# Performance work log

Measured on AMD Instinct MI355X. Metric: run time of the kernel, lower is better.

The kernel has to match this reference:

```python
import jax, jax.numpy as jnp
import numpy as np

NUM_HEADS = 32
NUM_KV = 8
HEAD_DIM = 128


def rotate_half(x):
    half = x.shape[-1] // 2
    x1, x2 = x[..., :half], x[..., half:]
    return jnp.concatenate([-x2, x1], axis=-1)


def apply_rope(x, cos, sin):
    # x: [B, H, S, D]; cos/sin: [S, D] broadcast over batch and heads
    return x * cos + rotate_half(x) * sin


def setup_inputs() -> dict:
    key = jax.random.key(0)
    kx, kqkv, kout = jax.random.split(key, 3)
    B, S, H = 2, 2048, 4096
    x = jax.random.normal(kx, (B, S, H), dtype=jnp.float32)
    Wqkv = jax.random.normal(kqkv, (H, NUM_HEADS * HEAD_DIM + 2 * NUM_KV * HEAD_DIM), dtype=jnp.float32) * (H ** -0.5)
    Wout = jax.random.normal(kout, (H, H), dtype=jnp.float32) * (H ** -0.5)
    # realistic RoPE tables (seq, head_dim)
    inv_freq = 1.0 / (10000.0 ** (np.arange(0, HEAD_DIM, 2, dtype=np.float32) / HEAD_DIM))
    freqs = np.outer(np.arange(S, dtype=np.float32), inv_freq)  # [S, D/2]
    emb = np.concatenate([freqs, freqs], axis=-1)  # [S, D]
    cos = jnp.asarray(np.cos(emb), dtype=jnp.float32)
    sin = jnp.asarray(np.sin(emb), dtype=jnp.float32)
    return {"x": x, "cos": cos, "sin": sin, "Wqkv": Wqkv, "Wout": Wout}


def reference(x, cos, sin, Wqkv, Wout):
    B, S, H = x.shape
    nh, nkv, hd = NUM_HEADS, NUM_KV, HEAD_DIM
    qkv = x @ Wqkv  # [B, S, (nh+2*nkv)*hd]
    q, k, v = jnp.split(qkv, [nh * hd, nh * hd + nkv * hd], axis=-1)
    q = q.reshape(B, S, nh, hd).transpose(0, 2, 1, 3)   # [B, nh, S, hd]
    k = k.reshape(B, S, nkv, hd).transpose(0, 2, 1, 3)  # [B, nkv, S, hd]
    v = v.reshape(B, S, nkv, hd).transpose(0, 2, 1, 3)
    q = apply_rope(q, cos, sin)
    k = apply_rope(k, cos, sin)
    group = nh // nkv
    k = jnp.repeat(k, group, axis=1)  # repeat_interleave over head dim
    v = jnp.repeat(v, group, axis=1)
    scale = 1.0 / jnp.sqrt(jnp.asarray(hd, dtype=x.dtype))
    scores = jnp.einsum('bhqd,bhkd->bhqk', q, k) * scale  # [B, nh, S, S]
    causal = jnp.triu(jnp.ones((S, S), dtype=bool), k=1)
    scores = jnp.where(causal, -jnp.inf, scores)
    w = jax.nn.softmax(scores, axis=-1)
    out = jnp.einsum('bhqk,bhkd->bhqd', w, v)  # [B, nh, S, hd]
    out = out.transpose(0, 2, 1, 3).reshape(B, S, nh * hd)
    return out @ Wout
```

## Files before the change

kernel.cpp:

```cpp
#include <hip/hip_runtime.h>

typedef unsigned short u16;
typedef __attribute__((ext_vector_type(8))) short s16x8;
typedef __attribute__((ext_vector_type(4))) short s16x4;
typedef __attribute__((ext_vector_type(4))) float f32x4;

#define DEVI __device__ __forceinline__

DEVI u16 f2b(float f) {
  union { float f; unsigned u; } v; v.f = f;
  unsigned r = v.u + 0x7FFFu + ((v.u >> 16) & 1u);
  return (u16)(r >> 16);
}
DEVI float b2f(u16 h) {
  union { unsigned u; float f; } v; v.u = ((unsigned)h) << 16;
  return v.f;
}

typedef const __attribute__((address_space(1))) void gas_void;
typedef __attribute__((address_space(3))) void las_void;
DEVI void gload16(const void* g, void* l) {
  __builtin_amdgcn_global_load_lds((gas_void*)g, (las_void*)l, 16, 0, 0);
}

__global__ void conv_bf16(const float* __restrict__ in, u16* __restrict__ out, int n8) {
  int i = blockIdx.x * 256 + threadIdx.x;
  if (i >= n8) return;
  const float* p = in + (size_t)i * 8;
  float4 u = *(const float4*)p;
  float4 v = *(const float4*)(p + 4);
  s16x8 o = {(short)f2b(u.x), (short)f2b(u.y), (short)f2b(u.z), (short)f2b(u.w),
             (short)f2b(v.x), (short)f2b(v.y), (short)f2b(v.z), (short)f2b(v.w)};
  *(s16x8*)(out + (size_t)i * 8) = o;
}

__global__ void trans_bf16(const float* __restrict__ W, u16* __restrict__ Wt, int K, int N) {
  __shared__ __attribute__((aligned(16))) u16 tile[64][68];
  const int t = threadIdx.x;
  const int n0 = blockIdx.x * 64, k0 = blockIdx.y * 64;
#pragma unroll
  for (int i = 0; i < 4; ++i) {
    int c = i * 256 + t;
    int r = c >> 4, q = c & 15;
    float4 v = *(const float4*)(W + (size_t)(k0 + r) * N + n0 + q * 4);
    s16x4 o = {(short)f2b(v.x), (short)f2b(v.y), (short)f2b(v.z), (short)f2b(v.w)};
    *(s16x4*)&tile[r][q * 4] = o;
  }
  __syncthreads();
#pragma unroll
  for (int i = 0; i < 2; ++i) {
    int c = i * 256 + t;
    int n_ = c >> 3, ck = (c & 7) * 8;
    s16x8 o;
#pragma unroll
    for (int j = 0; j < 8; ++j) o[j] = (short)tile[ck + j][n_];
    *(s16x8*)(Wt + (size_t)(n0 + n_) * K + k0 + ck) = o;
  }
}

template <typename TC>
__global__ __launch_bounds__(512, 2) void gemm128(const u16* __restrict__ A,
                                                  const u16* __restrict__ Bt,
                                                  TC* __restrict__ C, int M, int N, int K) {
  __shared__ __attribute__((aligned(16))) u16 As[2][128 * 64];
  __shared__ __attribute__((aligned(16))) u16 Bs[2][256 * 64];
  const int t = threadIdx.x;
  const int nbn = N >> 8;
  const int nwg = (M >> 7) * nbn;
  const int chunk = nwg >> 3;
  const int id = (blockIdx.x & 7) * chunk + (blockIdx.x >> 3);
  const int row0 = (id / nbn) << 7, col0 = (id % nbn) << 8;
  const int w = t >> 6, lane = t & 63, lc = lane & 15, lg = lane >> 4;
  const int wm = (w >> 2) * 64;
  const int wn4 = (w & 3);
  const int sw7 = lc & 7;

  const f32x4 FZ = {0.f, 0.f, 0.f, 0.f};
  f32x4 acc[4][4];
#pragma unroll
  for (int i = 0; i < 4; ++i)
#pragma unroll
    for (int j = 0; j < 4; ++j) acc[i][j] = FZ;

  const int ra = t >> 3;
  const int sa = (t & 7) ^ (ra & 7);
  const int bg0 = ((ra >> 5) << 6) | (ra & 31);

#define G1_STG_A(kt, sl)                                                          \
  {                                                                               \
    const u16* ap = A + (size_t)(row0 + ra) * K + ((kt) << 6) + (sa << 3);        \
    gload16(ap, (u16*)As[sl] + t * 8);                                            \
    gload16(ap + (size_t)64 * K, (u16*)As[sl] + (512 + t) * 8);                   \
  }
#define G1_STG_B(kt, H, sl)                                                       \
  {                                                                               \
    const u16* bp = Bt + (size_t)(col0 + bg0 + ((H) << 5)) * K + ((kt) << 6) + (sa << 3); \
    gload16(bp, (u16*)Bs[sl] + (H)*8192 + t * 8);                                 \
    gload16(bp + (size_t)128 * K, (u16*)Bs[sl] + (H)*8192 + (512 + t) * 8);       \
  }
#define G1_LOAD_A(buf)                                                            \
  _Pragma("unroll") for (int mf = 0; mf < 4; ++mf)                                \
  _Pragma("unroll") for (int ks = 0; ks < 2; ++ks)                                \
    af[mf][ks] = *(const s16x8*)(As[buf] + (wm + mf * 16 + lc) * 64 +             \
                                 (((ks * 4 + lg) ^ sw7) << 3));
#define G1_LOAD_B(NH, buf)                                                        \
  _Pragma("unroll") for (int nfl = 0; nfl < 2; ++nfl)                             \
  _Pragma("unroll") for (int ks = 0; ks < 2; ++ks)                                \
    bfv[nfl][ks] = *(const s16x8*)(Bs[buf] + ((NH)*128 + wn4 * 32 + nfl * 16 + lc) * 64 + \
                                   (((ks * 4 + lg) ^ sw7) << 3));
#define G1_MFMA(NH)                                                               \
  _Pragma("unroll") for (int ks = 0; ks < 2; ++ks)                                \
  _Pragma("unroll") for (int mf = 0; mf < 4; ++mf)                                \
  _Pragma("unroll") for (int nfl = 0; nfl < 2; ++nfl)                             \
    acc[mf][(NH)*2 + nfl] = __builtin_amdgcn_mfma_f32_16x16x32_bf16(              \
        af[mf][ks], bfv[nfl][ks], acc[mf][(NH)*2 + nfl], 0, 0, 0);
#define BAR __builtin_amdgcn_s_barrier()
#define PRIO1 __builtin_amdgcn_s_setprio(1)
#define PRIO0 __builtin_amdgcn_s_setprio(0)

  s16x8 af[4][2], bfv[2][2];
  const int NT = K >> 6, TM = NT - 1;

  G1_STG_A(0, 0) G1_STG_B(0, 0, 0) G1_STG_B(0, 1, 0)
  asm volatile("s_waitcnt vmcnt(2)" ::: "memory");
  BAR;

  for (int kt = 0; kt < NT; ++kt) {
    const int buf = kt & 1, nb = buf ^ 1;
    const int tp1 = (kt + 1) & TM;
    G1_LOAD_A(buf)
    G1_LOAD_B(0, buf)
    G1_STG_A(tp1, nb)
    G1_STG_B(tp1, 0, nb)
    BAR; PRIO1; G1_MFMA(0) PRIO0;
    asm volatile("s_waitcnt vmcnt(4)" ::: "memory");
    BAR;
    G1_LOAD_B(1, buf)
    G1_STG_B(tp1, 1, nb)
    BAR; PRIO1; G1_MFMA(1) PRIO0;
    asm volatile("s_waitcnt vmcnt(2)" ::: "memory");
    BAR;
  }
  asm volatile("s_waitcnt vmcnt(0)" ::: "memory");
#undef G1_STG_A
#undef G1_STG_B
#undef G1_LOAD_A
#undef G1_LOAD_B
#undef G1_MFMA
#undef BAR
#undef PRIO1
#undef PRIO0

#pragma unroll
  for (int mf = 0; mf < 4; ++mf)
#pragma unroll
    for (int nf = 0; nf < 4; ++nf)
#pragma unroll
      for (int r = 0; r < 4; ++r) {
        const int rg = row0 + wm + mf * 16 + lg * 4 + r;
        const int cg = col0 + wn4 * 64 + (nf >> 1) * 32 + (nf & 1) * 16 + lc;
        if constexpr (sizeof(TC) == 2)
          ((u16*)C)[(size_t)rg * N + cg] = f2b(acc[mf][nf][r]);
        else
          ((float*)C)[(size_t)rg * N + cg] = acc[mf][nf][r];
      }
}

template <typename TC>
__global__ __launch_bounds__(512, 2) void gemm256(const u16* __restrict__ A,
                                                  const u16* __restrict__ Bt,
                                                  TC* __restrict__ C, int M, int N, int K) {
  __shared__ __attribute__((aligned(16))) u16 As[2][2][128 * 64];
  __shared__ __attribute__((aligned(16))) u16 Bs[2][2][128 * 64];
  const int t = threadIdx.x;
  const int nbn = N >> 8;
  const int nwg = (M >> 8) * nbn;
  const int chunk = nwg >> 3;
  const int id = (blockIdx.x & 7) * chunk + (blockIdx.x >> 3);
  const int row0 = (id / nbn) << 8, col0 = (id % nbn) << 8;
  const int w = t >> 6, lane = t & 63, lc = lane & 15, lg = lane >> 4;
  const int wqm = (w >> 2) * 64;
  const int wqn = (w & 3) * 32;
  const int sw7 = lc & 7;

  const f32x4 FZ = {0.f, 0.f, 0.f, 0.f};
  f32x4 acc[4][4][2];
#pragma unroll
  for (int q = 0; q < 4; ++q)
#pragma unroll
    for (int i = 0; i < 4; ++i)
#pragma unroll
      for (int j = 0; j < 2; ++j) acc[q][i][j] = FZ;

  const int s_r0 = t >> 3, s_r1 = (512 + t) >> 3;
  const int s_s = t & 7;

#define STG_A(kt, H, sl)                                                                   \
  {                                                                                        \
    gload16(A + (size_t)(row0 + (H)*128 + s_r0) * K + ((kt) << 6) + ((s_s ^ (s_r0 & 7)) << 3), \
            (u16*)As[sl][H] + t * 8);                                                      \
    gload16(A + (size_t)(row0 + (H)*128 + s_r1) * K + ((kt) << 6) + ((s_s ^ (s_r1 & 7)) << 3), \
            (u16*)As[sl][H] + (512 + t) * 8);                                              \
  }
#define STG_B(kt, H, sl)                                                                   \
  {                                                                                        \
    gload16(Bt + (size_t)(col0 + (H)*128 + s_r0) * K + ((kt) << 6) + ((s_s ^ (s_r0 & 7)) << 3), \
            (u16*)Bs[sl][H] + t * 8);                                                      \
    gload16(Bt + (size_t)(col0 + (H)*128 + s_r1) * K + ((kt) << 6) + ((s_s ^ (s_r1 & 7)) << 3), \
            (u16*)Bs[sl][H] + (512 + t) * 8);                                              \
  }
#define LOAD_A(MH, buf)                                                           \
  _Pragma("unroll") for (int mf = 0; mf < 4; ++mf)                                \
  _Pragma("unroll") for (int ks = 0; ks < 2; ++ks)                                \
    af[mf][ks] = *(const s16x8*)(As[buf][MH] + (wqm + mf * 16 + lc) * 64 +        \
                                 (((ks * 4 + lg) ^ sw7) << 3));
#define LOAD_B(NH, buf, DST)                                                      \
  _Pragma("unroll") for (int nf = 0; nf < 2; ++nf)                                \
  _Pragma("unroll") for (int ks = 0; ks < 2; ++ks)                                \
    DST[nf][ks] = *(const s16x8*)(Bs[buf][NH] + (wqn + nf * 16 + lc) * 64 +       \
                                  (((ks * 4 + lg) ^ sw7) << 3));
#define MFMA_Q(q, BV)                                                             \
  _Pragma("unroll") for (int ks = 0; ks < 2; ++ks)                                \
  _Pragma("unroll") for (int mf = 0; mf < 4; ++mf)                                \
  _Pragma("unroll") for (int nf = 0; nf < 2; ++nf)                                \
    acc[q][mf][nf] = __builtin_amdgcn_mfma_f32_16x16x32_bf16(                     \
        af[mf][ks], BV[nf][ks], acc[q][mf][nf], 0, 0, 0);
#define BAR __builtin_amdgcn_s_barrier()
#define PRIO1 __builtin_amdgcn_s_setprio(1)
#define PRIO0 __builtin_amdgcn_s_setprio(0)
#define WAIT6 asm volatile("s_waitcnt vmcnt(6)" ::: "memory")

  s16x8 af[4][2], bfv0[2][2], bfv1[2][2];
  const int NT = K >> 6, TM = NT - 1;

  STG_A(0, 0, 0) STG_B(0, 0, 0) STG_B(0, 1, 0) STG_A(0, 1, 0)
  STG_A(1, 0, 1) STG_B(1, 0, 1) STG_B(1, 1, 1)
  WAIT6;
  BAR;

  for (int kt = 0; kt < NT; ++kt) {
    const int buf = kt & 1, nb = buf ^ 1;
    const int tp1 = (kt + 1) & TM, tp2 = (kt + 2) & TM;
    LOAD_A(0, buf) LOAD_B(0, buf, bfv0)
    STG_A(tp1, 1, nb)
    BAR; PRIO1; MFMA_Q(0, bfv0) PRIO0; BAR;
    LOAD_B(1, buf, bfv1)
    STG_A(tp2, 0, buf)
    BAR; PRIO1; MFMA_Q(1, bfv1) PRIO0; BAR;
    LOAD_A(1, buf)
    STG_B(tp2, 0, buf)
    BAR; PRIO1; MFMA_Q(2, bfv1) PRIO0; BAR;
    STG_B(tp2, 1, buf)
    BAR; PRIO1; MFMA_Q(3, bfv0) PRIO0;
    WAIT6;
    BAR;
  }
  asm volatile("s_waitcnt vmcnt(0)" ::: "memory");
  BAR;
#undef STG_A
#undef STG_B
#undef LOAD_A
#undef LOAD_B
#undef MFMA_Q
#undef BAR
#undef PRIO1
#undef PRIO0
#undef WAIT6

  const int qmh[4] = {0, 0, 1, 1}, qnh[4] = {0, 1, 1, 0};
#pragma unroll
  for (int q = 0; q < 4; ++q)
#pragma unroll
    for (int mf = 0; mf < 4; ++mf)
#pragma unroll
      for (int nf = 0; nf < 2; ++nf)
#pragma unroll
        for (int r = 0; r < 4; ++r) {
          const int rg = row0 + qmh[q] * 128 + wqm + mf * 16 + lg * 4 + r;
          const int cg = col0 + qnh[q] * 128 + wqn + nf * 16 + lc;
          if constexpr (sizeof(TC) == 2)
            ((u16*)C)[(size_t)rg * N + cg] = f2b(acc[q][mf][nf][r]);
          else
            ((float*)C)[(size_t)rg * N + cg] = acc[q][mf][nf][r];
        }
}

__global__ void rope_kernel(u16* __restrict__ qkv, const float* __restrict__ cosb,
                            const float* __restrict__ sinb) {
  const int bs = blockIdx.x;
  const int s = bs & 2047;
  u16* row = qkv + (size_t)bs * 6144;
  const float* cr = cosb + s * 128;
  const float* sr = sinb + s * 128;
  for (int p = threadIdx.x; p < 320; p += 256) {
    int head = p >> 3, dc = (p & 7) * 8;
    int ci = head * 128 + dc;
    s16x8 a = *(const s16x8*)&row[ci];
    s16x8 bb = *(const s16x8*)&row[ci + 64];
    float4 c0 = *(const float4*)(cr + dc), c1 = *(const float4*)(cr + dc + 4);
    float4 s0 = *(const float4*)(sr + dc), s1 = *(const float4*)(sr + dc + 4);
    float cv[8] = {c0.x, c0.y, c0.z, c0.w, c1.x, c1.y, c1.z, c1.w};
    float sv[8] = {s0.x, s0.y, s0.z, s0.w, s1.x, s1.y, s1.z, s1.w};
    s16x8 o1, o2;
#pragma unroll
    for (int j = 0; j < 8; ++j) {
      float x1 = b2f((u16)a[j]), x2 = b2f((u16)bb[j]);
      o1[j] = (short)f2b(x1 * cv[j] - x2 * sv[j]);
      o2[j] = (short)f2b(x2 * cv[j] + x1 * sv[j]);
    }
    *(s16x8*)&row[ci] = o1;
    *(s16x8*)&row[ci + 64] = o2;
  }
}

__global__ void vtrans_kernel(const u16* __restrict__ qkv, u16* __restrict__ v_t) {
  __shared__ __attribute__((aligned(16))) u16 tile[64][72];
  const int t = threadIdx.x;
  const int s0 = blockIdx.x * 64;
  const int d0 = blockIdx.y * 64;
  const int bk = blockIdx.z;
  const int b = bk >> 3, kvh = bk & 7;
  const int slot = t & 7, r0 = t >> 3;
#pragma unroll
  for (int i = 0; i < 2; ++i) {
    int s_ = r0 + 32 * i;
    *(s16x8*)&tile[s_][slot * 8] =
        *(const s16x8*)(qkv + (size_t)(b * 2048 + s0 + s_) * 6144 + 5120 + kvh * 128 + d0 + slot * 8);
  }
  __syncthreads();
#pragma unroll
  for (int i = 0; i < 2; ++i) {
    int d_ = r0 + 32 * i;
    s16x8 v;
#pragma unroll
    for (int j = 0; j < 8; ++j) v[j] = (short)tile[slot * 8 + j][d_];
    *(s16x8*)(v_t + ((size_t)bk * 128 + d0 + d_) * 2048 + s0 + slot * 8) = v;
  }
}

__global__ void __launch_bounds__(256, 2) attn_kernel(const u16* __restrict__ qkv,
                                                      const u16* __restrict__ v_t,
                                                      u16* __restrict__ attn) {
  __shared__ __attribute__((aligned(16))) u16 Ks[64][136];
  __shared__ __attribute__((aligned(16))) u16 Vs[128][72];
  __shared__ __attribute__((aligned(16))) u16 Ps[4][32][72];
  const int t = threadIdx.x;
  const int f = blockIdx.x;
  const int xcd = f & 7, ix = f >> 3;
  const int g = (xcd << 1) | (ix >> 6);
  const int r_ = ix & 63;
  const int b = g >> 3, kvh = g & 7;
  const int qt = 15 - (r_ >> 2);
  const int h = kvh * 4 + (r_ & 3);
  const int q0 = qt * 128;
  const int w = t >> 6, lane = t & 63, lc = lane & 15, lg = lane >> 4;
  const int qw = q0 + w * 32;

  const u16* qbase = qkv + (size_t)(b * 2048) * 6144 + h * 128;
  const u16* kbase = qkv + (size_t)(b * 2048) * 6144 + 4096 + kvh * 128;
  const u16* vbase = v_t + (size_t)(b * 8 + kvh) * 128 * 2048;

  s16x8 qf[2][4];
#pragma unroll
  for (int mf = 0; mf < 2; ++mf)
#pragma unroll
    for (int ks = 0; ks < 4; ++ks)
      qf[mf][ks] = *(const s16x8*)(qbase + (size_t)(qw + mf * 16 + lc) * 6144 + ks * 32 + lg * 8);

  const f32x4 FZ = {0.f, 0.f, 0.f, 0.f};
  f32x4 o_acc[2][8];
  float m_run[2][4], l_run[2][4];
#pragma unroll
  for (int mf = 0; mf < 2; ++mf) {
#pragma unroll
    for (int nf = 0; nf < 8; ++nf) o_acc[mf][nf] = FZ;
#pragma unroll
    for (int r = 0; r < 4; ++r) { m_run[mf][r] = -3e38f; l_run[mf][r] = 0.f; }
  }
  const float scale2 = 0.08838834764831845f * 1.44269504088896340736f;

  const int ntiles = q0 / 64 + 2;
  s16x8 kr[4], vr[4];
#pragma unroll
  for (int i = 0; i < 4; ++i) {
    int c = i * 256 + t;
    kr[i] = *(const s16x8*)(kbase + (size_t)(c >> 4) * 6144 + (c & 15) * 8);
    vr[i] = *(const s16x8*)(vbase + (size_t)(c >> 3) * 2048 + (c & 7) * 8);
  }

  for (int kt = 0; kt < ntiles; ++kt) {
    const int k0 = kt * 64;
    __syncthreads();
#pragma unroll
    for (int i = 0; i < 4; ++i) {
      int c = i * 256 + t;
      *(s16x8*)&Ks[c >> 4][(c & 15) * 8] = kr[i];
      *(s16x8*)&Vs[c >> 3][(c & 7) * 8] = vr[i];
    }
    __syncthreads();
    if (kt + 1 < ntiles) {
      int k1 = k0 + 64;
#pragma unroll
      for (int i = 0; i < 4; ++i) {
        int c = i * 256 + t;
        kr[i] = *(const s16x8*)(kbase + (size_t)(k1 + (c >> 4)) * 6144 + (c & 15) * 8);
        vr[i] = *(const s16x8*)(vbase + (size_t)(c >> 3) * 2048 + k1 + (c & 7) * 8);
      }
    }
    if (k0 > qw + 31) continue;

    f32x4 sacc[2][4];
#pragma unroll
    for (int mf = 0; mf < 2; ++mf)
#pragma unroll
      for (int nf = 0; nf < 4; ++nf) sacc[mf][nf] = FZ;
#pragma unroll
    for (int ks = 0; ks < 4; ++ks) {
      s16x8 kf[4];
#pragma unroll
      for (int nf = 0; nf < 4; ++nf)
        kf[nf] = *(const s16x8*)&Ks[nf * 16 + lc][ks * 32 + lg * 8];
#pragma unroll
      for (int mf = 0; mf < 2; ++mf)
#pragma unroll
        for (int nf = 0; nf < 4; ++nf)
          sacc[mf][nf] = __builtin_amdgcn_mfma_f32_16x16x32_bf16(qf[mf][ks], kf[nf], sacc[mf][nf], 0, 0, 0);
    }

#pragma unroll
    for (int mf = 0; mf < 2; ++mf) {
      float pm[4] = {-3e38f, -3e38f, -3e38f, -3e38f};
      const bool dm = (k0 + 63 > qw + mf * 16);
      if (dm) {
#pragma unroll
        for (int nf = 0; nf < 4; ++nf) {
          int kv = k0 + nf * 16 + lc;
#pragma unroll
          for (int r = 0; r < 4; ++r) {
            int qg = qw + mf * 16 + lg * 4 + r;
            float sv = sacc[mf][nf][r] * scale2;
            sv = (kv <= qg) ? sv : -3e38f;
            sacc[mf][nf][r] = sv;
            pm[r] = fmaxf(pm[r], sv);
          }
        }
      } else {
#pragma unroll
        for (int nf = 0; nf < 4; ++nf)
#pragma unroll
          for (int r = 0; r < 4; ++r) {
            float sv = sacc[mf][nf][r] * scale2;
            sacc[mf][nf][r] = sv;
            pm[r] = fmaxf(pm[r], sv);
          }
      }
#pragma unroll
      for (int r = 0; r < 4; ++r) {
        pm[r] = fmaxf(pm[r], __shfl_xor(pm[r], 1));
        pm[r] = fmaxf(pm[r], __shfl_xor(pm[r], 2));
        pm[r] = fmaxf(pm[r], __shfl_xor(pm[r], 4));
        pm[r] = fmaxf(pm[r], __shfl_xor(pm[r], 8));
      }
      bool any = false;
      float mnew[4];
#pragma unroll
      for (int r = 0; r < 4; ++r) {
        mnew[r] = fmaxf(m_run[mf][r], pm[r]);
        any |= (mnew[r] > m_run[mf][r]);
      }
      if (__any(any)) {
#pragma unroll
        for (int r = 0; r < 4; ++r) {
          float fsc = exp2f(m_run[mf][r] - mnew[r]);
          m_run[mf][r] = mnew[r];
          l_run[mf][r] *= fsc;
#pragma unroll
          for (int nf = 0; nf < 8; ++nf) o_acc[mf][nf][r] *= fsc;
        }
      }
      float psum[4] = {0.f, 0.f, 0.f, 0.f};
#pragma unroll
      for (int nf = 0; nf < 4; ++nf)
#pragma unroll
        for (int r = 0; r < 4; ++r) {
          float p = exp2f(sacc[mf][nf][r] - m_run[mf][r]);
          psum[r] += p;
          Ps[w][mf * 16 + lg * 4 + r][nf * 16 + lc] = f2b(p);
        }
#pragma unroll
      for (int r = 0; r < 4; ++r) {
        float ps = psum[r];
        ps += __shfl_xor(ps, 1);
        ps += __shfl_xor(ps, 2);
        ps += __shfl_xor(ps, 4);
        ps += __shfl_xor(ps, 8);
        l_run[mf][r] += ps;
      }
    }
#pragma unroll
    for (int ks = 0; ks < 2; ++ks) {
      s16x8 pf[2];
#pragma unroll
      for (int mf = 0; mf < 2; ++mf)
        pf[mf] = *(const s16x8*)&Ps[w][mf * 16 + lc][ks * 32 + lg * 8];
#pragma unroll
      for (int nf = 0; nf < 8; ++nf) {
        s16x8 vf = *(const s16x8*)&Vs[nf * 16 + lc][ks * 32 + lg * 8];
#pragma unroll
        for (int mf = 0; mf < 2; ++mf)
          o_acc[mf][nf] = __builtin_amdgcn_mfma_f32_16x16x32_bf16(pf[mf], vf, o_acc[mf][nf], 0, 0, 0);
      }
    }
  }

#pragma unroll
  for (int mf = 0; mf < 2; ++mf)
#pragma unroll
    for (int r = 0; r < 4; ++r) {
      float inv = 1.0f / l_run[mf][r];
      int qg = qw + mf * 16 + lg * 4 + r;
#pragma unroll
      for (int nf = 0; nf < 8; ++nf)
        attn[(size_t)(b * 2048 + qg) * 4096 + h * 128 + nf * 16 + lc] =
            f2b(o_acc[mf][nf][r] * inv);
    }
}

extern "C" void kernel_launch(void* const* d_in, const int* in_sizes, int n_in,
                              void* d_out, int out_size, void* d_ws, size_t ws_size,
                              hipStream_t stream) {
  (void)in_sizes; (void)n_in; (void)out_size; (void)ws_size;
  const float* x = (const float*)d_in[0];
  const float* cosb = (const float*)d_in[1];
  const float* sinb = (const float*)d_in[2];
  const float* Wqkv = (const float*)d_in[3];
  const float* Wout = (const float*)d_in[4];
  float* out = (float*)d_out;
  char* ws = (char*)d_ws;

  u16* buf0 = (u16*)ws;
  u16* buf1 = (u16*)(ws + 50331648);
  u16* regc = (u16*)(ws + 100663296);

  conv_bf16<<<8192, 256, 0, stream>>>(x, regc, 2097152);
  trans_bf16<<<dim3(96, 64), 256, 0, stream>>>(Wqkv, buf0, 4096, 6144);
  gemm128<u16><<<768, 512, 0, stream>>>(regc, buf0, buf1, 4096, 6144, 4096);
  rope_kernel<<<4096, 256, 0, stream>>>(buf1, cosb, sinb);
  vtrans_kernel<<<dim3(32, 2, 16), 256, 0, stream>>>(buf1, regc);
  attn_kernel<<<1024, 256, 0, stream>>>(buf1, regc, buf0);
  trans_bf16<<<dim3(64, 64), 256, 0, stream>>>(Wout, regc, 4096, 4096);
  gemm256<float><<<256, 512, 0, stream>>>(buf0, regc, out, 4096, 4096, 4096);
}
```

Baseline: 564.7 us.

## Triple-buffer LDS tiles in GEMM to prefetch two k-steps ahead

Result: no change. 563.9 us (-0.1%).

```diff
diff --git a/kernel.cpp b/kernel.cpp
--- a/kernel.cpp
+++ b/kernel.cpp
@@ -62,8 +62,8 @@
 __global__ __launch_bounds__(512, 2) void gemm128(const u16* __restrict__ A,
                                                   const u16* __restrict__ Bt,
                                                   TC* __restrict__ C, int M, int N, int K) {
-  __shared__ __attribute__((aligned(16))) u16 As[2][128 * 64];
-  __shared__ __attribute__((aligned(16))) u16 Bs[2][256 * 64];
+  __shared__ __attribute__((aligned(16))) u16 As[3 * 128 * 64];
+  __shared__ __attribute__((aligned(16))) u16 Bs[3 * 256 * 64];
   const int t = threadIdx.x;
   const int nbn = N >> 8;
   const int nwg = (M >> 7) * nbn;
@@ -86,27 +86,27 @@
   const int sa = (t & 7) ^ (ra & 7);
   const int bg0 = ((ra >> 5) << 6) | (ra & 31);
 
-#define G1_STG_A(kt, sl)                                                          \
+#define G1_STG_A(kt, AP)                                                          \
   {                                                                               \
     const u16* ap = A + (size_t)(row0 + ra) * K + ((kt) << 6) + (sa << 3);        \
-    gload16(ap, (u16*)As[sl] + t * 8);                                            \
-    gload16(ap + (size_t)64 * K, (u16*)As[sl] + (512 + t) * 8);                   \
-  }
-#define G1_STG_B(kt, H, sl)                                                       \
+    gload16(ap, (AP) + t * 8);                                                    \
+    gload16(ap + (size_t)64 * K, (AP) + (512 + t) * 8);                           \
+  }
+#define G1_STG_B(kt, H, BP)                                                       \
   {                                                                               \
     const u16* bp = Bt + (size_t)(col0 + bg0 + ((H) << 5)) * K + ((kt) << 6) + (sa << 3); \
-    gload16(bp, (u16*)Bs[sl] + (H)*8192 + t * 8);                                 \
-    gload16(bp + (size_t)128 * K, (u16*)Bs[sl] + (H)*8192 + (512 + t) * 8);       \
-  }
-#define G1_LOAD_A(buf)                                                            \
+    gload16(bp, (BP) + (H)*8192 + t * 8);                                         \
+    gload16(bp + (size_t)128 * K, (BP) + (H)*8192 + (512 + t) * 8);               \
+  }
+#define G1_LOAD_A(AP)                                                             \
   _Pragma("unroll") for (int mf = 0; mf < 4; ++mf)                                \
   _Pragma("unroll") for (int ks = 0; ks < 2; ++ks)                                \
-    af[mf][ks] = *(const s16x8*)(As[buf] + (wm + mf * 16 + lc) * 64 +             \
+    af[mf][ks] = *(const s16x8*)((AP) + (wm + mf * 16 + lc) * 64 +                \
                                  (((ks * 4 + lg) ^ sw7) << 3));
-#define G1_LOAD_B(NH, buf)                                                        \
+#define G1_LOAD_B(NH, BP)                                                         \
   _Pragma("unroll") for (int nfl = 0; nfl < 2; ++nfl)                             \
   _Pragma("unroll") for (int ks = 0; ks < 2; ++ks)                                \
-    bfv[nfl][ks] = *(const s16x8*)(Bs[buf] + ((NH)*128 + wn4 * 32 + nfl * 16 + lc) * 64 + \
+    bfv[nfl][ks] = *(const s16x8*)((BP) + ((NH)*128 + wn4 * 32 + nfl * 16 + lc) * 64 + \
                                    (((ks * 4 + lg) ^ sw7) << 3));
 #define G1_MFMA(NH)                                                               \
   _Pragma("unroll") for (int ks = 0; ks < 2; ++ks)                                \
@@ -121,25 +121,28 @@
   s16x8 af[4][2], bfv[2][2];
   const int NT = K >> 6, TM = NT - 1;
 
-  G1_STG_A(0, 0) G1_STG_B(0, 0, 0) G1_STG_B(0, 1, 0)
-  asm volatile("s_waitcnt vmcnt(2)" ::: "memory");
+  u16 *Ac = As, *An = As + 8192, *Ap = As + 16384;
+  u16 *Bc = Bs, *Bn = Bs + 16384, *Bp = Bs + 32768;
+
+  G1_STG_A(0, Ac) G1_STG_B(0, 0, Bc) G1_STG_B(0, 1, Bc)
+  G1_STG_A(1, An) G1_STG_B(1, 0, Bn) G1_STG_B(1, 1, Bn)
+  asm volatile("s_waitcnt vmcnt(6)" ::: "memory");
   BAR;
 
   for (int kt = 0; kt < NT; ++kt) {
-    const int buf = kt & 1, nb = buf ^ 1;
-    const int tp1 = (kt + 1) & TM;
-    G1_LOAD_A(buf)
-    G1_LOAD_B(0, buf)
-    G1_STG_A(tp1, nb)
-    G1_STG_B(tp1, 0, nb)
-    BAR; PRIO1; G1_MFMA(0) PRIO0;
-    asm volatile("s_waitcnt vmcnt(4)" ::: "memory");
+    const int tp2 = (kt + 2) & TM;
+    G1_LOAD_A(Ac)
+    G1_LOAD_B(0, Bc)
+    G1_STG_A(tp2, Ap)
+    G1_STG_B(tp2, 0, Bp)
+    BAR; PRIO1; G1_MFMA(0) PRIO0; BAR;
+    G1_LOAD_B(1, Bc)
+    G1_STG_B(tp2, 1, Bp)
+    BAR; PRIO1; G1_MFMA(1) PRIO0;
+    asm volatile("s_waitcnt vmcnt(6)" ::: "memory");
     BAR;
-    G1_LOAD_B(1, buf)
-    G1_STG_B(tp1, 1, nb)
-    BAR; PRIO1; G1_MFMA(1) PRIO0;
-    asm volatile("s_waitcnt vmcnt(2)" ::: "memory");
-    BAR;
+    u16* ta = Ac; Ac = An; An = Ap; Ap = ta;
+    u16* tb = Bc; Bc = Bn; Bn = Bp; Bp = tb;
   }
   asm volatile("s_waitcnt vmcnt(0)" ::: "memory");
 #undef G1_STG_A
```
